# Optimization experiments

Hardware: AMD Instinct MI355X
Metric: run time of the kernel (lower is better)

Reference implementation:

```python
import jax, jax.numpy as jnp
import numpy as np

B, L, N = 32, 64, 8
C, H_IMG, W_IMG = 3, 40, 40
HID = 64
N_ACT = 8
CNN_OUT = 64  # 64 channels * 1 * 1 spatial after the three convs on 40x40


def _conv(x, w, b, stride):
    # x: (B', Cin, H, W), w: (Cout, Cin, kh, kw)
    y = jax.lax.conv_general_dilated(
        x, w, window_strides=(stride, stride), padding='VALID',
        dimension_numbers=('NCHW', 'OIHW', 'NCHW'))
    return y + b[None, :, None, None]


def setup_inputs() -> dict:
    key = jax.random.key(0)
    ks = jax.random.split(key, 12)

    def rn(k, shape, fan_in):
        return jax.random.normal(k, shape, dtype=jnp.float32) * (1.0 / np.sqrt(fan_in))

    inp = {
        'obs_batch': jax.random.normal(ks[0], (B, L, N, C, H_IMG, W_IMG), dtype=jnp.float32),
        'hidden_state': jnp.zeros((B, N, HID), dtype=jnp.float32),
        'conv1_w': rn(ks[1], (32, C, 8, 8), C * 8 * 8),
        'conv1_b': jnp.zeros((32,), jnp.float32),
        'conv2_w': rn(ks[2], (64, 32, 4, 4), 32 * 4 * 4),
        'conv2_b': jnp.zeros((64,), jnp.float32),
        'conv3_w': rn(ks[3], (64, 64, 3, 3), 64 * 3 * 3),
        'conv3_b': jnp.zeros((64,), jnp.float32),
        'w_ih': rn(ks[4], (3 * HID, CNN_OUT), CNN_OUT),
        'w_hh': rn(ks[5], (3 * HID, HID), HID),
        'b_ih': jnp.zeros((3 * HID,), jnp.float32),
        'b_hh': jnp.zeros((3 * HID,), jnp.float32),
        'fc_w': rn(ks[6], (N_ACT, HID), HID),
        'fc_b': jnp.zeros((N_ACT,), jnp.float32),
    }
    return inp


def reference(obs_batch, hidden_state, conv1_w, conv1_b, conv2_w, conv2_b,
              conv3_w, conv3_b, w_ih, w_hh, b_ih, b_hh, fc_w, fc_b):
    b, l, n = obs_batch.shape[:3]
    x = obs_batch.reshape(-1, C, H_IMG, W_IMG)            # (B*L*N, C, H, W)
    x = jax.nn.relu(_conv(x, conv1_w, conv1_b, 4))
    x = jax.nn.relu(_conv(x, conv2_w, conv2_b, 2))
    x = jax.nn.relu(_conv(x, conv3_w, conv3_b, 1))
    feats = x.reshape(b, l, n, -1)                        # (B, L, N, F)

    # (L, B*N, F) time-major for scan
    rnn_in = feats.transpose(1, 0, 2, 3).reshape(l, b * n, -1)
    h0 = hidden_state.reshape(b * n, HID)

    def step(h, xt):
        gi = xt @ w_ih.T + b_ih
        gh = h @ w_hh.T + b_hh
        i_r, i_z, i_n = jnp.split(gi, 3, axis=-1)
        h_r, h_z, h_n = jnp.split(gh, 3, axis=-1)
        r = jax.nn.sigmoid(i_r + h_r)
        z = jax.nn.sigmoid(i_z + h_z)
        nn_ = jnp.tanh(i_n + r * h_n)
        h_new = (1.0 - z) * nn_ + z * h
        return h_new, h_new

    h_last, hs = jax.lax.scan(step, h0, rnn_in)           # hs: (L, B*N, HID)

    # torch path: stack (L, B*N, H) -> permute to (B*N, L, H) -> reshape (B*L*N, H)
    rnn_out = hs.transpose(1, 0, 2).reshape(b, n, l, HID).transpose(0, 2, 1, 3)
    q = rnn_out.reshape(-1, HID) @ fc_w.T + fc_b
    q_values = q.reshape(b, l, n, N_ACT)
    next_hidden_state = h_last.reshape(b, n, HID)
    return q_values, next_hidden_state
```

## Files before the change

kernel.cpp:

```cpp
#include <hip/hip_runtime.h>
#include <math.h>

typedef unsigned short ushort_t;
typedef unsigned int uint_t;
typedef __attribute__((ext_vector_type(8))) short short8_t;
typedef __attribute__((ext_vector_type(4))) float f32x4_t;

constexpr int Bb = 32, Ll = 64, Nn = 8;
constexpr int IMGS = Bb * Ll * Nn;
constexpr int Cc = 3, Hh = 40, Ww = 40;
constexpr int HID = 64, G3 = 192, NACT = 8;

__device__ inline float bf2f(ushort_t u) {
  union { uint_t i; float f; } v; v.i = ((uint_t)u) << 16; return v.f;
}
__device__ inline ushort_t f2bf(float f) {
  union { float f; uint_t u; } v; v.f = f;
  uint_t r = v.u + 0x7fffu + ((v.u >> 16) & 1u);
  return (ushort_t)(r >> 16);
}
__device__ inline void unpack2(uint_t u, float& lo, float& hi) {
  union { uint_t i; float f; } a, b;
  a.i = u << 16; b.i = u & 0xffff0000u;
  lo = a.f; hi = b.f;
}
__device__ inline float ld1(const void* p, int idx, int isbf) {
  return isbf ? bf2f(((const ushort_t*)p)[idx]) : ((const float*)p)[idx];
}
__device__ inline short8_t ldsh8(const ushort_t* p) {
  union { short8_t v; uint2 u[2]; } r;
  r.u[0] = *(const uint2*)p;
  r.u[1] = *(const uint2*)(p + 4);
  return r.v;
}
__device__ inline short8_t ldg8(const ushort_t* p) {
  union { short8_t v; uint4 u; } r;
  r.u = *(const uint4*)p;
  return r.v;
}
#define WAVE_FENCE() asm volatile("s_waitcnt lgkmcnt(0)" ::: "memory")

__global__ __launch_bounds__(256) void detect_kernel(
    const ushort_t* __restrict__ obs, const ushort_t* __restrict__ whh,
    int* __restrict__ flags) {
  __shared__ int cnt[2];
  if (threadIdx.x < 2) cnt[threadIdx.x] = 0;
  __syncthreads();
  int bad0 = 0, bad1 = 0;
  for (int i = threadIdx.x; i < 4096; i += 256) {
    int e0 = (obs[i] >> 7) & 0xFF; if (e0 >= 0xC0) bad0++;
    int e1 = (whh[i] >> 7) & 0xFF; if (e1 >= 0xC0) bad1++;
  }
  atomicAdd(&cnt[0], bad0);
  atomicAdd(&cnt[1], bad1);
  __syncthreads();
  if (threadIdx.x == 0) { flags[0] = (cnt[0] <= 4); flags[1] = (cnt[1] <= 4); }
}

__global__ __launch_bounds__(256) void repack_kernel(
    const void* __restrict__ w1, const void* __restrict__ w2,
    const void* __restrict__ w3, const void* __restrict__ wih,
    const int* __restrict__ flags,
    ushort_t* __restrict__ w1pack, ushort_t* __restrict__ w2pack,
    ushort_t* __restrict__ w3bf, ushort_t* __restrict__ wihb) {
  const int fw = flags[1];
  int t = blockIdx.x * 256 + threadIdx.x;
  if (t < 6144) w1pack[t] = f2bf(ld1(w1, t, fw));
  if (t < 32768) {
    int oc = t >> 9, r = t & 511;
    int kykx = r >> 5, ic = r & 31;
    w2pack[t] = f2bf(ld1(w2, oc * 512 + ic * 16 + kykx, fw));
  }
  if (t < 36864) w3bf[t] = f2bf(ld1(w3, t, fw));
  if (t < 12288) wihb[t] = f2bf(ld1(wih, t, fw));
}

__global__ __launch_bounds__(256, 4) void conv12_kernel(
    const void* __restrict__ obs, const ushort_t* __restrict__ w1pack,
    const ushort_t* __restrict__ w2pack,
    const void* __restrict__ b1, const void* __restrict__ b2,
    const int* __restrict__ flags, ushort_t* __restrict__ f2g, int img_base) {
  __shared__ __attribute__((aligned(16))) ushort_t s_mem[4][4800];

  const int tid = threadIdx.x;
  const int wave = tid >> 6, lane = tid & 63;
  const int lrow = lane & 15, lk8 = lane >> 4;
  const int fobs = flags[0], fw = flags[1];
  const int img0 = blockIdx.x * 4;

  if (fobs) {
    const uint4* src = reinterpret_cast<const uint4*>((const ushort_t*)obs + ((size_t)img_base + img0) * 4800);
    uint4 r[10];
#pragma unroll
    for (int it = 0; it < 10; ++it) {
      const int i = it * 256 + tid;
      r[it] = src[i < 2400 ? i : 2399];
    }
#pragma unroll
    for (int it = 0; it < 10; ++it) {
      const int i = it * 256 + tid;
      if (i < 2400) {
        const int im_ = i / 600, e = i - im_ * 600;
        reinterpret_cast<uint4*>(s_mem[im_])[e] = r[it];
      }
    }
  } else {
    const float4* src = reinterpret_cast<const float4*>((const float*)obs + ((size_t)img_base + img0) * 4800);
#pragma unroll
    for (int bb = 0; bb < 2; ++bb) {
      float4 r[10];
#pragma unroll
      for (int it = 0; it < 10; ++it) {
        const int i = (bb * 10 + it) * 256 + tid;
        r[it] = src[i < 4800 ? i : 4799];
      }
#pragma unroll
      for (int it = 0; it < 10; ++it) {
        const int i = (bb * 10 + it) * 256 + tid;
        if (i < 4800) {
          const int im_ = i / 1200, e = i - im_ * 1200;
          uint2 o;
          o.x = (uint_t)f2bf(r[it].x) | ((uint_t)f2bf(r[it].y) << 16);
          o.y = (uint_t)f2bf(r[it].z) | ((uint_t)f2bf(r[it].w) << 16);
          reinterpret_cast<uint2*>(s_mem[im_])[e] = o;
        }
      }
    }
  }
  __syncthreads();

  {
    ushort_t* si = s_mem[wave];
    int ab[6];
#pragma unroll
    for (int mt = 0; mt < 6; ++mt) {
      int p = mt * 16 + lrow; if (p > 80) p = 80;
      ab[mt] = (p / 9) * 160 + (p % 9) * 4;
    }
    f32x4_t acc[2][6];
#pragma unroll
    for (int nt = 0; nt < 2; ++nt)
#pragma unroll
      for (int mt = 0; mt < 6; ++mt) acc[nt][mt] = (f32x4_t){0.f, 0.f, 0.f, 0.f};
    const ushort_t* wr0 = w1pack + lrow * 192 + lk8 * 8;
#pragma unroll
    for (int ks = 0; ks < 6; ++ks) {
      const int g = ks * 4 + lk8;
      const int aoff = (g >> 3) * 1600 + (g & 7) * 40;
      short8_t b0 = ldg8(wr0 + ks * 32);
      short8_t b1v = ldg8(wr0 + 16 * 192 + ks * 32);
#pragma unroll
      for (int mt = 0; mt < 6; ++mt) {
        short8_t a = ldsh8(&si[aoff + ab[mt]]);
        acc[0][mt] = __builtin_amdgcn_mfma_f32_16x16x32_bf16(a, b0, acc[0][mt], 0, 0, 0);
        acc[1][mt] = __builtin_amdgcn_mfma_f32_16x16x32_bf16(a, b1v, acc[1][mt], 0, 0, 0);
      }
    }
    WAVE_FENCE();
    const float bz0 = ld1(b1, lrow, fw), bz1 = ld1(b1, 16 + lrow, fw);
#pragma unroll
    for (int mt = 0; mt < 6; ++mt) {
#pragma unroll
      for (int r = 0; r < 4; ++r) {
        const int p = mt * 16 + lk8 * 4 + r;
        if (p < 81) {
          si[p * 40 + lrow]      = f2bf(fmaxf(acc[0][mt][r] + bz0, 0.f));
          si[p * 40 + 16 + lrow] = f2bf(fmaxf(acc[1][mt][r] + bz1, 0.f));
        }
      }
    }
  }
  __syncthreads();

  {
    int imgr[3], pbx[3];
#pragma unroll
    for (int mt = 0; mt < 3; ++mt) {
      int row = mt * 16 + lrow; if (row > 35) row = 35;
      const int ir = row / 9, p2 = row - ir * 9;
      imgr[mt] = ir;
      pbx[mt] = (p2 / 3) * 18 + (p2 % 3) * 2;
    }
    f32x4_t acc[3];
#pragma unroll
    for (int mt = 0; mt < 3; ++mt) acc[mt] = (f32x4_t){0.f, 0.f, 0.f, 0.f};
    const ushort_t* w2r = w2pack + (wave * 16 + lrow) * 512 + lk8 * 8;
#pragma unroll
    for (int s = 0; s < 16; ++s) {
      const int po = (s >> 2) * 9 + (s & 3);
      short8_t bv = ldg8(w2r + s * 32);
      short8_t a0 = ldsh8(&s_mem[imgr[0]][(pbx[0] + po) * 40 + lk8 * 8]);
      short8_t a1 = ldsh8(&s_mem[imgr[1]][(pbx[1] + po) * 40 + lk8 * 8]);
      short8_t a2 = ldsh8(&s_mem[imgr[2]][(pbx[2] + po) * 40 + lk8 * 8]);
      acc[0] = __builtin_amdgcn_mfma_f32_16x16x32_bf16(a0, bv, acc[0], 0, 0, 0);
      acc[1] = __builtin_amdgcn_mfma_f32_16x16x32_bf16(a1, bv, acc[1], 0, 0, 0);
      acc[2] = __builtin_amdgcn_mfma_f32_16x16x32_bf16(a2, bv, acc[2], 0, 0, 0);
    }
    const int oc = wave * 16 + lrow;
    const float bias = ld1(b2, oc, fw);
#pragma unroll
    for (int mt = 0; mt < 3; ++mt) {
#pragma unroll
      for (int r = 0; r < 4; ++r) {
        const int row = mt * 16 + lk8 * 4 + r;
        if (row < 36) {
          const int ir = row / 9, pp = row - ir * 9;
          f2g[((size_t)img_base + img0 + ir) * 576 + oc * 9 + pp] =
              f2bf(fmaxf(acc[mt][r] + bias, 0.f));
        }
      }
    }
  }
}

__global__ __launch_bounds__(256) void conv3gi_kernel(
    const ushort_t* __restrict__ f2g, const ushort_t* __restrict__ w3bf,
    const ushort_t* __restrict__ wihb, const void* __restrict__ b3,
    const int* __restrict__ flags, float* __restrict__ gi, int img_base) {
  __shared__ __attribute__((aligned(16))) ushort_t f2b[16 * 592];
  __shared__ __attribute__((aligned(16))) ushort_t f3b[16 * 72];

  const int tid = threadIdx.x;
  const int wave = tid >> 6, lane = tid & 63;
  const int lrow = lane & 15, lk8 = lane >> 4;
  const int fw = flags[1];
  const int iloc0 = blockIdx.x * 16;

  for (int i = tid; i < 16 * 72; i += 256) {
    const int im_ = i / 72, off = i - im_ * 72;
    *reinterpret_cast<uint4*>(&f2b[im_ * 592 + off * 8]) =
        *reinterpret_cast<const uint4*>(&f2g[((size_t)img_base + iloc0 + im_) * 576 + off * 8]);
  }
  __syncthreads();

  {
    f32x4_t c3 = (f32x4_t){0.f, 0.f, 0.f, 0.f};
    const ushort_t* w3r = w3bf + (wave * 16 + lrow) * 576 + lk8 * 8;
#pragma unroll
    for (int ks = 0; ks < 18; ++ks) {
      short8_t a = ldsh8(&f2b[lrow * 592 + ks * 32 + lk8 * 8]);
      short8_t bv = ldg8(w3r + ks * 32);
      c3 = __builtin_amdgcn_mfma_f32_16x16x32_bf16(a, bv, c3, 0, 0, 0);
    }
    const int oc = wave * 16 + lrow;
    const float bias = ld1(b3, oc, fw);
#pragma unroll
    for (int r = 0; r < 4; ++r)
      f3b[(lk8 * 4 + r) * 72 + oc] = f2bf(fmaxf(c3[r] + bias, 0.f));
  }
  __syncthreads();

#pragma unroll
  for (int t = 0; t < 3; ++t) {
    const int nt = wave * 3 + t;
    f32x4_t g = (f32x4_t){0.f, 0.f, 0.f, 0.f};
#pragma unroll
    for (int ks = 0; ks < 2; ++ks) {
      short8_t a = ldsh8(&f3b[lrow * 72 + ks * 32 + lk8 * 8]);
      short8_t bv = ldg8(wihb + (nt * 16 + lrow) * 64 + ks * 32 + lk8 * 8);
      g = __builtin_amdgcn_mfma_f32_16x16x32_bf16(a, bv, g, 0, 0, 0);
    }
#pragma unroll
    for (int r = 0; r < 4; ++r)
      gi[((size_t)img_base + iloc0 + lk8 * 4 + r) * G3 + nt * 16 + lrow] = g[r];
  }
}

__global__ __launch_bounds__(64, 1) void gru_kernel(
    const float* __restrict__ gi, const void* __restrict__ h0,
    const void* __restrict__ whh, const void* __restrict__ bih,
    const void* __restrict__ bhh, const int* __restrict__ flags,
    float* __restrict__ rnn, float* __restrict__ hout) {
  __shared__ float s_h[HID];
  const int j = threadIdx.x;
  const int s = blockIdx.x;
  const int fw = flags[1];

  float4 wr[16], wz[16], wn[16];
  if (fw) {
    const uint4* wb = reinterpret_cast<const uint4*>(whh);
#pragma unroll
    for (int i = 0; i < 8; ++i) {
      uint4 a = wb[(size_t)j * 8 + i];
      unpack2(a.x, wr[2 * i].x, wr[2 * i].y);
      unpack2(a.y, wr[2 * i].z, wr[2 * i].w);
      unpack2(a.z, wr[2 * i + 1].x, wr[2 * i + 1].y);
      unpack2(a.w, wr[2 * i + 1].z, wr[2 * i + 1].w);
      uint4 b = wb[(size_t)(64 + j) * 8 + i];
      unpack2(b.x, wz[2 * i].x, wz[2 * i].y);
      unpack2(b.y, wz[2 * i].z, wz[2 * i].w);
      unpack2(b.z, wz[2 * i + 1].x, wz[2 * i + 1].y);
      unpack2(b.w, wz[2 * i + 1].z, wz[2 * i + 1].w);
      uint4 c = wb[(size_t)(128 + j) * 8 + i];
      unpack2(c.x, wn[2 * i].x, wn[2 * i].y);
      unpack2(c.y, wn[2 * i].z, wn[2 * i].w);
      unpack2(c.z, wn[2 * i + 1].x, wn[2 * i + 1].y);
      unpack2(c.w, wn[2 * i + 1].z, wn[2 * i + 1].w);
    }
  } else {
    const float4* wf = reinterpret_cast<const float4*>(whh);
#pragma unroll
    for (int i = 0; i < 16; ++i) {
      wr[i] = wf[(size_t)j * 16 + i];
      wz[i] = wf[(size_t)(64 + j) * 16 + i];
      wn[i] = wf[(size_t)(128 + j) * 16 + i];
    }
  }

  float h = ld1(h0, s * HID + j, fw);
  s_h[j] = h;
  const float bir = ld1(bih, j, fw), biz = ld1(bih, 64 + j, fw), bin_ = ld1(bih, 128 + j, fw);
  const float bhr = ld1(bhh, j, fw), bhz = ld1(bhh, 64 + j, fw), bhn = ld1(bhh, 128 + j, fw);
  const int b = s >> 3, n = s & 7;
  const float* gbase = gi + ((size_t)b * Ll * Nn + n) * G3;
  float* rbase = rnn + ((size_t)b * Ll * Nn + n) * HID;
  WAVE_FENCE();

  float g0 = gbase[j], g1 = gbase[64 + j], g2 = gbase[128 + j];

  for (int l = 0; l < Ll; ++l) {
    float p0 = 0.f, p1 = 0.f, p2 = 0.f;
    if (l + 1 < Ll) {
      const float* gn = gbase + (size_t)(l + 1) * Nn * G3;
      p0 = gn[j]; p1 = gn[64 + j]; p2 = gn[128 + j];
    }
    float hr = bhr, hz = bhz, hn = bhn;
#pragma unroll
    for (int k = 0; k < 16; ++k) {
      float4 hv = *reinterpret_cast<const float4*>(&s_h[k * 4]);
      hr += wr[k].x * hv.x + wr[k].y * hv.y + wr[k].z * hv.z + wr[k].w * hv.w;
      hz += wz[k].x * hv.x + wz[k].y * hv.y + wz[k].z * hv.z + wz[k].w * hv.w;
      hn += wn[k].x * hv.x + wn[k].y * hv.y + wn[k].z * hv.z + wn[k].w * hv.w;
    }
    const float gr = g0 + bir + hr;
    const float gz = g1 + biz + hz;
    const float gn_ = g2 + bin_;
    const float r = 1.f / (1.f + __expf(-gr));
    const float z = 1.f / (1.f + __expf(-gz));
    const float nn_ = tanhf(gn_ + r * hn);
    h = (1.f - z) * nn_ + z * h;
    WAVE_FENCE();
    s_h[j] = h;
    rbase[(size_t)l * Nn * HID + j] = h;
    WAVE_FENCE();
    g0 = p0; g1 = p1; g2 = p2;
  }
  hout[(size_t)s * HID + j] = h;
}

__global__ __launch_bounds__(64) void fc_kernel(
    const float* __restrict__ rnn, const void* __restrict__ fcw,
    const void* __restrict__ fcb, const int* __restrict__ flags,
    float* __restrict__ q) {
  __shared__ float s_w[NACT * HID];
  __shared__ float s_b[NACT];
  const int tid = threadIdx.x;
  const int fw = flags[1];
  for (int i = tid; i < NACT * HID; i += 64) s_w[i] = ld1(fcw, i, fw);
  if (tid < NACT) s_b[tid] = ld1(fcb, tid, fw);
  __syncthreads();
  const int row = blockIdx.x * 64 + tid;
  float x[64];
  const float4* xp = reinterpret_cast<const float4*>(rnn + (size_t)row * HID);
#pragma unroll
  for (int i = 0; i < 16; ++i) {
    float4 v = xp[i];
    x[4 * i] = v.x; x[4 * i + 1] = v.y; x[4 * i + 2] = v.z; x[4 * i + 3] = v.w;
  }
#pragma unroll
  for (int a = 0; a < NACT; ++a) {
    float v = s_b[a];
#pragma unroll
    for (int k = 0; k < 64; ++k) v += x[k] * s_w[a * 64 + k];
    q[(size_t)row * NACT + a] = v;
  }
}

extern "C" void kernel_launch(void* const* d_in, const int* in_sizes, int n_in,
                              void* d_out, int out_size, void* d_ws, size_t ws_size,
                              hipStream_t stream) {
  const void* obs = d_in[0];
  const void* h0  = d_in[1];
  const void* w1  = d_in[2];
  const void* b1  = d_in[3];
  const void* w2  = d_in[4];
  const void* b2  = d_in[5];
  const void* w3  = d_in[6];
  const void* b3  = d_in[7];
  const void* wih = d_in[8];
  const void* whh = d_in[9];
  const void* bih = d_in[10];
  const void* bhh = d_in[11];
  const void* fcw = d_in[12];
  const void* fcb = d_in[13];

  float* qout = (float*)d_out;
  float* hout = qout + (size_t)IMGS * NACT;

  char* wsb = (char*)d_ws;
  int*      flags  = (int*)wsb;
  float*    gi     = (float*)(wsb + 16);
  float*    rnn    = gi + (size_t)IMGS * G3;
  ushort_t* w1pack = (ushort_t*)(rnn + (size_t)IMGS * HID);
  ushort_t* w2pack = w1pack + 6144;
  ushort_t* w3bf   = w2pack + 32768;
  ushort_t* wihb   = w3bf + 36864;
  ushort_t* f2g    = wihb + 12288;

  const size_t base_bytes = (size_t)((char*)f2g - wsb);
  size_t cap = (ws_size > base_bytes) ? (ws_size - base_bytes) / 1152 : 0;
  cap = (cap / 16) * 16;
  if (cap > (size_t)IMGS) cap = IMGS;

  detect_kernel<<<1, 256, 0, stream>>>((const ushort_t*)obs, (const ushort_t*)whh, flags);
  repack_kernel<<<144, 256, 0, stream>>>(w1, w2, w3, wih, flags, w1pack, w2pack, w3bf, wihb);

  for (int c0 = 0; c0 < IMGS; c0 += (int)cap) {
    int n = IMGS - c0; if (n > (int)cap) n = (int)cap;
    conv12_kernel<<<n / 4, 256, 0, stream>>>(obs, w1pack, w2pack, b1, b2, flags, f2g, c0);
    conv3gi_kernel<<<n / 16, 256, 0, stream>>>(f2g, w3bf, wihb, b3, flags, gi, c0);
  }

  gru_kernel<<<256, 64, 0, stream>>>(gi, h0, whh, bih, bhh, flags, rnn, hout);
  fc_kernel<<<IMGS / 64, 64, 0, stream>>>(rnn, fcw, fcb, flags, qout);
}
```

Measured before the change: 202.3 us.

## Make conv12 persistent with double-buffered LDS prefetch of next image tile

Turns conv12 into a persistent kernel with a fixed grid of 512 blocks. Each block loops over image tiles and prefetches the next tile's observations into registers while the current tile's MFMAs run, then writes them into a second LDS buffer. The conv1 weights and biases are hoisted into registers once per block, and the conv2 output is staged through LDS so it can be written to global memory as coalesced 16-byte stores. The workspace chunking loop is dropped, so f2g is assumed to hold all images. The cost is doubled LDS, lower occupancy (launch bounds 2) and more register pressure from the prefetch buffers.

```diff
diff --git a/kernel.cpp b/kernel.cpp
--- a/kernel.cpp
+++ b/kernel.cpp
@@ -10,6 +10,9 @@
 constexpr int IMGS = Bb * Ll * Nn;
 constexpr int Cc = 3, Hh = 40, Ww = 40;
 constexpr int HID = 64, G3 = 192, NACT = 8;
+constexpr int CGRID = 512;
+constexpr int NTILE = IMGS / 4;
+constexpr int NITER = NTILE / CGRID;
 
 __device__ inline float bf2f(ushort_t u) {
   union { uint_t i; float f; } v; v.i = ((uint_t)u) << 16; return v.f;
@@ -75,141 +78,218 @@
   if (t < 12288) wihb[t] = f2bf(ld1(wih, t, fw));
 }
 
-__global__ __launch_bounds__(256, 4) void conv12_kernel(
+__global__ __launch_bounds__(256, 2) void conv12_kernel(
     const void* __restrict__ obs, const ushort_t* __restrict__ w1pack,
     const ushort_t* __restrict__ w2pack,
     const void* __restrict__ b1, const void* __restrict__ b2,
-    const int* __restrict__ flags, ushort_t* __restrict__ f2g, int img_base) {
-  __shared__ __attribute__((aligned(16))) ushort_t s_mem[4][4800];
+    const int* __restrict__ flags, ushort_t* __restrict__ f2g) {
+  __shared__ __attribute__((aligned(16))) ushort_t s_mem[2][4][4800];
 
   const int tid = threadIdx.x;
   const int wave = tid >> 6, lane = tid & 63;
   const int lrow = lane & 15, lk8 = lane >> 4;
   const int fobs = flags[0], fw = flags[1];
-  const int img0 = blockIdx.x * 4;
-
-  if (fobs) {
-    const uint4* src = reinterpret_cast<const uint4*>((const ushort_t*)obs + ((size_t)img_base + img0) * 4800);
-    uint4 r[10];
-#pragma unroll
-    for (int it = 0; it < 10; ++it) {
-      const int i = it * 256 + tid;
-      r[it] = src[i < 2400 ? i : 2399];
-    }
-#pragma unroll
-    for (int it = 0; it < 10; ++it) {
-      const int i = it * 256 + tid;
-      if (i < 2400) {
-        const int im_ = i / 600, e = i - im_ * 600;
-        reinterpret_cast<uint4*>(s_mem[im_])[e] = r[it];
-      }
-    }
-  } else {
-    const float4* src = reinterpret_cast<const float4*>((const float*)obs + ((size_t)img_base + img0) * 4800);
-#pragma unroll
-    for (int bb = 0; bb < 2; ++bb) {
-      float4 r[10];
+
+  short8_t wb0[6], wb1[6];
+  {
+    const ushort_t* wr0 = w1pack + lrow * 192 + lk8 * 8;
+#pragma unroll
+    for (int ks = 0; ks < 6; ++ks) {
+      wb0[ks] = ldg8(wr0 + ks * 32);
+      wb1[ks] = ldg8(wr0 + 16 * 192 + ks * 32);
+    }
+  }
+  const float bz0 = ld1(b1, lrow, fw), bz1 = ld1(b1, 16 + lrow, fw);
+
+  int ab[6];
+#pragma unroll
+  for (int mt = 0; mt < 6; ++mt) {
+    int p = mt * 16 + lrow; if (p > 80) p = 80;
+    ab[mt] = (p / 9) * 160 + (p % 9) * 4;
+  }
+  int imgr[3], pbx[3];
+#pragma unroll
+  for (int mt = 0; mt < 3; ++mt) {
+    int row = mt * 16 + lrow; if (row > 35) row = 35;
+    const int ir = row / 9, p2 = row - ir * 9;
+    imgr[mt] = ir;
+    pbx[mt] = (p2 / 3) * 18 + (p2 % 3) * 2;
+  }
+  const ushort_t* w2r = w2pack + (wave * 16 + lrow) * 512 + lk8 * 8;
+  const float b2v = ld1(b2, wave * 16 + lrow, fw);
+
+  {
+    const int img0 = blockIdx.x * 4;
+    if (fobs) {
+      const uint4* src = reinterpret_cast<const uint4*>((const ushort_t*)obs + (size_t)img0 * 4800);
+      uint4 r[10];
+#pragma unroll
+      for (int it = 0; it < 10; ++it) { const int i = it * 256 + tid; r[it] = src[i < 2400 ? i : 2399]; }
 #pragma unroll
       for (int it = 0; it < 10; ++it) {
-        const int i = (bb * 10 + it) * 256 + tid;
-        r[it] = src[i < 4800 ? i : 4799];
-      }
-#pragma unroll
-      for (int it = 0; it < 10; ++it) {
-        const int i = (bb * 10 + it) * 256 + tid;
-        if (i < 4800) {
-          const int im_ = i / 1200, e = i - im_ * 1200;
-          uint2 o;
-          o.x = (uint_t)f2bf(r[it].x) | ((uint_t)f2bf(r[it].y) << 16);
-          o.y = (uint_t)f2bf(r[it].z) | ((uint_t)f2bf(r[it].w) << 16);
-          reinterpret_cast<uint2*>(s_mem[im_])[e] = o;
-        }
-      }
-    }
-  }
-  __syncthreads();
-
-  {
-    ushort_t* si = s_mem[wave];
-    int ab[6];
-#pragma unroll
-    for (int mt = 0; mt < 6; ++mt) {
-      int p = mt * 16 + lrow; if (p > 80) p = 80;
-      ab[mt] = (p / 9) * 160 + (p % 9) * 4;
-    }
-    f32x4_t acc[2][6];
-#pragma unroll
-    for (int nt = 0; nt < 2; ++nt)
-#pragma unroll
-      for (int mt = 0; mt < 6; ++mt) acc[nt][mt] = (f32x4_t){0.f, 0.f, 0.f, 0.f};
-    const ushort_t* wr0 = w1pack + lrow * 192 + lk8 * 8;
-#pragma unroll
-    for (int ks = 0; ks < 6; ++ks) {
-      const int g = ks * 4 + lk8;
-      const int aoff = (g >> 3) * 1600 + (g & 7) * 40;
-      short8_t b0 = ldg8(wr0 + ks * 32);
-      short8_t b1v = ldg8(wr0 + 16 * 192 + ks * 32);
+        const int i = it * 256 + tid;
+        if (i < 2400) { const int im_ = i / 600, e = i - im_ * 600;
+          reinterpret_cast<uint4*>(s_mem[0][im_])[e] = r[it]; }
+      }
+    } else {
+      const float4* src = reinterpret_cast<const float4*>((const float*)obs + (size_t)img0 * 4800);
+#pragma unroll
+      for (int bb = 0; bb < 2; ++bb) {
+        float4 r[10];
+#pragma unroll
+        for (int it = 0; it < 10; ++it) { const int i = (bb * 10 + it) * 256 + tid; r[it] = src[i < 4800 ? i : 4799]; }
+#pragma unroll
+        for (int it = 0; it < 10; ++it) {
+          const int i = (bb * 10 + it) * 256 + tid;
+          if (i < 4800) {
+            const int im_ = i / 1200, e = i - im_ * 1200;
+            uint2 o;
+            o.x = (uint_t)f2bf(r[it].x) | ((uint_t)f2bf(r[it].y) << 16);
+            o.y = (uint_t)f2bf(r[it].z) | ((uint_t)f2bf(r[it].w) << 16);
+            reinterpret_cast<uint2*>(s_mem[0][im_])[e] = o;
+          }
+        }
+      }
+    }
+  }
+  __syncthreads();
+
+  for (int it = 0; it < NITER; ++it) {
+    const int c = it & 1;
+    const int tile = blockIdx.x + it * CGRID;
+    const int img0 = tile * 4;
+    const bool has_next = (it + 1 < NITER);
+    const size_t nbase = has_next ? (size_t)(blockIdx.x + (it + 1) * CGRID) * 4 * 4800 : 0;
+
+    uint4 rb16[10];
+    float4 rf0[10];
+    if (has_next) {
+      if (fobs) {
+        const uint4* src = reinterpret_cast<const uint4*>((const ushort_t*)obs + nbase);
+#pragma unroll
+        for (int t2 = 0; t2 < 10; ++t2) { const int i = t2 * 256 + tid; rb16[t2] = src[i < 2400 ? i : 2399]; }
+      } else {
+        const float4* src = reinterpret_cast<const float4*>((const float*)obs + nbase);
+#pragma unroll
+        for (int t2 = 0; t2 < 10; ++t2) { const int i = t2 * 256 + tid; rf0[t2] = src[i < 4800 ? i : 4799]; }
+      }
+    }
+
+    {
+      ushort_t* si = s_mem[c][wave];
+      f32x4_t acc[2][6];
+#pragma unroll
+      for (int nt = 0; nt < 2; ++nt)
+#pragma unroll
+        for (int mt = 0; mt < 6; ++mt) acc[nt][mt] = (f32x4_t){0.f, 0.f, 0.f, 0.f};
+#pragma unroll
+      for (int ks = 0; ks < 6; ++ks) {
+        const int g = ks * 4 + lk8;
+        const int aoff = (g >> 3) * 1600 + (g & 7) * 40;
+#pragma unroll
+        for (int mt = 0; mt < 6; ++mt) {
+          short8_t a = ldsh8(&si[aoff + ab[mt]]);
+          acc[0][mt] = __builtin_amdgcn_mfma_f32_16x16x32_bf16(a, wb0[ks], acc[0][mt], 0, 0, 0);
+          acc[1][mt] = __builtin_amdgcn_mfma_f32_16x16x32_bf16(a, wb1[ks], acc[1][mt], 0, 0, 0);
+        }
+      }
+      WAVE_FENCE();
 #pragma unroll
       for (int mt = 0; mt < 6; ++mt) {
-        short8_t a = ldsh8(&si[aoff + ab[mt]]);
-        acc[0][mt] = __builtin_amdgcn_mfma_f32_16x16x32_bf16(a, b0, acc[0][mt], 0, 0, 0);
-        acc[1][mt] = __builtin_amdgcn_mfma_f32_16x16x32_bf16(a, b1v, acc[1][mt], 0, 0, 0);
-      }
-    }
-    WAVE_FENCE();
-    const float bz0 = ld1(b1, lrow, fw), bz1 = ld1(b1, 16 + lrow, fw);
-#pragma unroll
-    for (int mt = 0; mt < 6; ++mt) {
-#pragma unroll
-      for (int r = 0; r < 4; ++r) {
-        const int p = mt * 16 + lk8 * 4 + r;
-        if (p < 81) {
-          si[p * 40 + lrow]      = f2bf(fmaxf(acc[0][mt][r] + bz0, 0.f));
-          si[p * 40 + 16 + lrow] = f2bf(fmaxf(acc[1][mt][r] + bz1, 0.f));
-        }
-      }
-    }
-  }
-  __syncthreads();
-
-  {
-    int imgr[3], pbx[3];
-#pragma unroll
-    for (int mt = 0; mt < 3; ++mt) {
-      int row = mt * 16 + lrow; if (row > 35) row = 35;
-      const int ir = row / 9, p2 = row - ir * 9;
-      imgr[mt] = ir;
-      pbx[mt] = (p2 / 3) * 18 + (p2 % 3) * 2;
-    }
-    f32x4_t acc[3];
-#pragma unroll
-    for (int mt = 0; mt < 3; ++mt) acc[mt] = (f32x4_t){0.f, 0.f, 0.f, 0.f};
-    const ushort_t* w2r = w2pack + (wave * 16 + lrow) * 512 + lk8 * 8;
-#pragma unroll
-    for (int s = 0; s < 16; ++s) {
-      const int po = (s >> 2) * 9 + (s & 3);
-      short8_t bv = ldg8(w2r + s * 32);
-      short8_t a0 = ldsh8(&s_mem[imgr[0]][(pbx[0] + po) * 40 + lk8 * 8]);
-      short8_t a1 = ldsh8(&s_mem[imgr[1]][(pbx[1] + po) * 40 + lk8 * 8]);
-      short8_t a2 = ldsh8(&s_mem[imgr[2]][(pbx[2] + po) * 40 + lk8 * 8]);
-      acc[0] = __builtin_amdgcn_mfma_f32_16x16x32_bf16(a0, bv, acc[0], 0, 0, 0);
-      acc[1] = __builtin_amdgcn_mfma_f32_16x16x32_bf16(a1, bv, acc[1], 0, 0, 0);
-      acc[2] = __builtin_amdgcn_mfma_f32_16x16x32_bf16(a2, bv, acc[2], 0, 0, 0);
-    }
-    const int oc = wave * 16 + lrow;
-    const float bias = ld1(b2, oc, fw);
-#pragma unroll
-    for (int mt = 0; mt < 3; ++mt) {
-#pragma unroll
-      for (int r = 0; r < 4; ++r) {
-        const int row = mt * 16 + lk8 * 4 + r;
-        if (row < 36) {
-          const int ir = row / 9, pp = row - ir * 9;
-          f2g[((size_t)img_base + img0 + ir) * 576 + oc * 9 + pp] =
-              f2bf(fmaxf(acc[mt][r] + bias, 0.f));
-        }
-      }
-    }
+#pragma unroll
+        for (int r = 0; r < 4; ++r) {
+          const int p = mt * 16 + lk8 * 4 + r;
+          if (p < 81) {
+            si[p * 40 + lrow]      = f2bf(fmaxf(acc[0][mt][r] + bz0, 0.f));
+            si[p * 40 + 16 + lrow] = f2bf(fmaxf(acc[1][mt][r] + bz1, 0.f));
+          }
+        }
+      }
+    }
+
+    float4 rf1[10];
+    if (has_next && !fobs) {
+      const float4* src = reinterpret_cast<const float4*>((const float*)obs + nbase);
+#pragma unroll
+      for (int t2 = 0; t2 < 10; ++t2) { const int i = (10 + t2) * 256 + tid; rf1[t2] = src[i < 4800 ? i : 4799]; }
+    }
+    __syncthreads();
+
+    {
+      f32x4_t acc[3];
+#pragma unroll
+      for (int mt = 0; mt < 3; ++mt) acc[mt] = (f32x4_t){0.f, 0.f, 0.f, 0.f};
+#pragma unroll
+      for (int s = 0; s < 16; ++s) {
+        const int po = (s >> 2) * 9 + (s & 3);
+        short8_t bv = ldg8(w2r + s * 32);
+        short8_t a0 = ldsh8(&s_mem[c][imgr[0]][(pbx[0] + po) * 40 + lk8 * 8]);
+        short8_t a1 = ldsh8(&s_mem[c][imgr[1]][(pbx[1] + po) * 40 + lk8 * 8]);
+        short8_t a2 = ldsh8(&s_mem[c][imgr[2]][(pbx[2] + po) * 40 + lk8 * 8]);
+        acc[0] = __builtin_amdgcn_mfma_f32_16x16x32_bf16(a0, bv, acc[0], 0, 0, 0);
+        acc[1] = __builtin_amdgcn_mfma_f32_16x16x32_bf16(a1, bv, acc[1], 0, 0, 0);
+        acc[2] = __builtin_amdgcn_mfma_f32_16x16x32_bf16(a2, bv, acc[2], 0, 0, 0);
+      }
+      const int oc = wave * 16 + lrow;
+#pragma unroll
+      for (int mt = 0; mt < 3; ++mt) {
+#pragma unroll
+        for (int r = 0; r < 4; ++r) {
+          const int row = mt * 16 + lk8 * 4 + r;
+          if (row < 36) {
+            const int ir = row / 9, pp = row - ir * 9;
+            s_mem[c][ir][3232 + oc * 9 + pp] = f2bf(fmaxf(acc[mt][r] + b2v, 0.f));
+          }
+        }
+      }
+    }
+    __syncthreads();
+
+#pragma unroll
+    for (int t2 = 0; t2 < 2; ++t2) {
+      const int i = t2 * 256 + tid;
+      if (i < 288) {
+        const int im_ = i / 72, off = i - im_ * 72;
+        *reinterpret_cast<uint4*>(&f2g[(size_t)(img0 + im_) * 576 + off * 8]) =
+            *reinterpret_cast<const uint4*>(&s_mem[c][im_][3232 + off * 8]);
+      }
+    }
+
+    if (has_next) {
+      const int nc = c ^ 1;
+      if (fobs) {
+#pragma unroll
+        for (int t2 = 0; t2 < 10; ++t2) {
+          const int i = t2 * 256 + tid;
+          if (i < 2400) { const int im_ = i / 600, e = i - im_ * 600;
+            reinterpret_cast<uint4*>(s_mem[nc][im_])[e] = rb16[t2]; }
+        }
+      } else {
+#pragma unroll
+        for (int t2 = 0; t2 < 10; ++t2) {
+          const int i = t2 * 256 + tid;
+          if (i < 4800) {
+            const int im_ = i / 1200, e = i - im_ * 1200;
+            uint2 o;
+            o.x = (uint_t)f2bf(rf0[t2].x) | ((uint_t)f2bf(rf0[t2].y) << 16);
+            o.y = (uint_t)f2bf(rf0[t2].z) | ((uint_t)f2bf(rf0[t2].w) << 16);
+            reinterpret_cast<uint2*>(s_mem[nc][im_])[e] = o;
+          }
+        }
+#pragma unroll
+        for (int t2 = 0; t2 < 10; ++t2) {
+          const int i = (10 + t2) * 256 + tid;
+          if (i < 4800) {
+            const int im_ = i / 1200, e = i - im_ * 1200;
+            uint2 o;
+            o.x = (uint_t)f2bf(rf1[t2].x) | ((uint_t)f2bf(rf1[t2].y) << 16);
+            o.y = (uint_t)f2bf(rf1[t2].z) | ((uint_t)f2bf(rf1[t2].w) << 16);
+            reinterpret_cast<uint2*>(s_mem[nc][im_])[e] = o;
+          }
+        }
+      }
+    }
+    __syncthreads();
   }
 }
 
@@ -407,19 +487,11 @@
   ushort_t* wihb   = w3bf + 36864;
   ushort_t* f2g    = wihb + 12288;
 
-  const size_t base_bytes = (size_t)((char*)f2g - wsb);
-  size_t cap = (ws_size > base_bytes) ? (ws_size - base_bytes) / 1152 : 0;
-  cap = (cap / 16) * 16;
-  if (cap > (size_t)IMGS) cap = IMGS;
-
   detect_kernel<<<1, 256, 0, stream>>>((const ushort_t*)obs, (const ushort_t*)whh, flags);
   repack_kernel<<<144, 256, 0, stream>>>(w1, w2, w3, wih, flags, w1pack, w2pack, w3bf, wihb);
 
-  for (int c0 = 0; c0 < IMGS; c0 += (int)cap) {
-    int n = IMGS - c0; if (n > (int)cap) n = (int)cap;
-    conv12_kernel<<<n / 4, 256, 0, stream>>>(obs, w1pack, w2pack, b1, b2, flags, f2g, c0);
-    conv3gi_kernel<<<n / 16, 256, 0, stream>>>(f2g, w3bf, wihb, b3, flags, gi, c0);
-  }
+  conv12_kernel<<<CGRID, 256, 0, stream>>>(obs, w1pack, w2pack, b1, b2, flags, f2g);
+  conv3gi_kernel<<<IMGS / 16, 256, 0, stream>>>(f2g, w3bf, wihb, b3, flags, gi, 0);
 
   gru_kernel<<<256, 64, 0, stream>>>(gi, h0, whh, bih, bhh, flags, rnn, hout);
   fc_kernel<<<IMGS / 64, 64, 0, stream>>>(rnn, fcw, fcb, flags, qout);
```

After: 252.9 us. 25.1% more time.
